# Performance work log

Hardware: AMD Instinct MI355X
Metric: run time of the kernel (lower is better)

## Reference

```python
import jax, jax.numpy as jnp
import numpy as np

NEG_SLOPE = 0.01  # torch nn.LeakyReLU default


def setup_inputs() -> dict:
    key = jax.random.key(0)
    k1, k2, k3, k4, k5 = jax.random.split(key, 5)
    B, C, N, O = 32, 512, 1024, 512
    x = jax.random.normal(k1, (B, C, N), dtype=jnp.float32)
    wq = jax.random.normal(k2, (C,), dtype=jnp.float32) * (1.0 / np.sqrt(C))
    wk = jax.random.normal(k3, (C,), dtype=jnp.float32) * (1.0 / np.sqrt(C))
    wm = jax.random.normal(k4, (O, C), dtype=jnp.float32) * (1.0 / np.sqrt(C))
    bm = jax.random.normal(k5, (O,), dtype=jnp.float32) * 0.01
    return {"x": x, "wq": wq, "wk": wk, "wm": wm, "bm": bm}


def reference(x, wq, wk, wm, bm):
    # x: [B, C, N]
    q = jnp.einsum('c,bcn->bn', wq, x)            # [B, N] (Conv1d C->1, k=1, no bias)
    k = jnp.einsum('c,bcn->bn', wk, x)            # [B, N]
    scores = q[:, None, :] + k[:, :, None]        # [B, N, N] additive broadcast
    scores = jnp.where(scores > 0, scores, NEG_SLOPE * scores)  # LeakyReLU
    att = jax.nn.softmax(scores, axis=-1)         # softmax over last dim
    agg = jnp.einsum('bcn,bmn->bcm', x, att)      # weighted aggregation [B, C, N]
    out = jnp.einsum('oc,bcm->bom', wm, agg) + bm[None, :, None]  # Conv1d k=1
    return jax.nn.relu(out)
```

## Files before the change

### kernel.cpp

```cpp
#include <hip/hip_runtime.h>


constexpr int B = 32, C = 512, N = 1024, O = 512;
constexpr float L2E = 1.4426950408889634f;

typedef _Float16 half8 __attribute__((ext_vector_type(8)));
typedef _Float16 half4v __attribute__((ext_vector_type(4)));
typedef _Float16 half2v __attribute__((ext_vector_type(2)));
typedef float f32x4 __attribute__((ext_vector_type(4)));
typedef float f32x16 __attribute__((ext_vector_type(16)));

#if __has_builtin(__builtin_amdgcn_exp2f)
#define EXP2(x) __builtin_amdgcn_exp2f(x)
#else
#define EXP2(x) exp2f(x)
#endif

__device__ __forceinline__ half8 cvt8(float4 a, float4 b) {
  half8 h;
  h[0] = (_Float16)a.x; h[1] = (_Float16)a.y; h[2] = (_Float16)a.z; h[3] = (_Float16)a.w;
  h[4] = (_Float16)b.x; h[5] = (_Float16)b.y; h[6] = (_Float16)b.z; h[7] = (_Float16)b.w;
  return h;
}

__device__ __forceinline__ void gload16(const _Float16* g, _Float16* l) {
  __builtin_amdgcn_global_load_lds(
      (const __attribute__((address_space(1))) unsigned int*)(g),
      (__attribute__((address_space(3))) unsigned int*)(l), 16, 0, 0);
}

__global__ __launch_bounds__(256) void prep_kernel(const float* __restrict__ x,
    const float* __restrict__ wq, const float* __restrict__ wk,
    const float* __restrict__ wm,
    float* __restrict__ q, float* __restrict__ k,
    _Float16* __restrict__ wmh, _Float16* __restrict__ xhT) {
  __shared__ half2v Ts[32 * 67];
  int b  = blockIdx.y;
  int n0 = blockIdx.x * 64;
  int t = threadIdx.x;

  if (blockIdx.x == 0) {
    const float* wsrc = wm + b * 8192;
    _Float16* wdst = wmh + b * 8192;
#pragma unroll
    for (int j = 0; j < 4; ++j) {
      int i = j * 2048 + t * 8;
      float4 a = *(const float4*)(wsrc + i);
      float4 bb = *(const float4*)(wsrc + i + 4);
      *(half8*)(wdst + i) = cvt8(a, bb);
    }
  }

  int cp = t >> 3;
  int ng = t & 7;
  const float* xbase = x + ((size_t)b * C + 2 * cp) * N + n0 + ng * 8;
  int nl = t >> 2;
  int hq = t & 3;
  _Float16* xout = xhT + ((size_t)b * N + n0 + nl) * C + hq * 16;
  float aq[8] = {}, ak[8] = {};

  for (int ch = 0; ch < 8; ++ch) {
    int c0 = ch * 64;
    const float* xr = xbase + (size_t)c0 * N;
    float4 a0 = *(const float4*)(xr);
    float4 a1 = *(const float4*)(xr + 4);
    float4 b0 = *(const float4*)(xr + N);
    float4 b1 = *(const float4*)(xr + N + 4);
    float2 wq2 = *(const float2*)&wq[c0 + 2 * cp];
    float2 wk2 = *(const float2*)&wk[c0 + 2 * cp];
    aq[0] = fmaf(wq2.x, a0.x, fmaf(wq2.y, b0.x, aq[0]));
    aq[1] = fmaf(wq2.x, a0.y, fmaf(wq2.y, b0.y, aq[1]));
    aq[2] = fmaf(wq2.x, a0.z, fmaf(wq2.y, b0.z, aq[2]));
    aq[3] = fmaf(wq2.x, a0.w, fmaf(wq2.y, b0.w, aq[3]));
    aq[4] = fmaf(wq2.x, a1.x, fmaf(wq2.y, b1.x, aq[4]));
    aq[5] = fmaf(wq2.x, a1.y, fmaf(wq2.y, b1.y, aq[5]));
    aq[6] = fmaf(wq2.x, a1.z, fmaf(wq2.y, b1.z, aq[6]));
    aq[7] = fmaf(wq2.x, a1.w, fmaf(wq2.y, b1.w, aq[7]));
    ak[0] = fmaf(wk2.x, a0.x, fmaf(wk2.y, b0.x, ak[0]));
    ak[1] = fmaf(wk2.x, a0.y, fmaf(wk2.y, b0.y, ak[1]));
    ak[2] = fmaf(wk2.x, a0.z, fmaf(wk2.y, b0.z, ak[2]));
    ak[3] = fmaf(wk2.x, a0.w, fmaf(wk2.y, b0.w, ak[3]));
    ak[4] = fmaf(wk2.x, a1.x, fmaf(wk2.y, b1.x, ak[4]));
    ak[5] = fmaf(wk2.x, a1.y, fmaf(wk2.y, b1.y, ak[5]));
    ak[6] = fmaf(wk2.x, a1.z, fmaf(wk2.y, b1.z, ak[6]));
    ak[7] = fmaf(wk2.x, a1.w, fmaf(wk2.y, b1.w, ak[7]));
    {
      half2v* xp = &Ts[cp * 67 + ng * 8];
      xp[0] = half2v{(_Float16)a0.x, (_Float16)b0.x};
      xp[1] = half2v{(_Float16)a0.y, (_Float16)b0.y};
      xp[2] = half2v{(_Float16)a0.z, (_Float16)b0.z};
      xp[3] = half2v{(_Float16)a0.w, (_Float16)b0.w};
      xp[4] = half2v{(_Float16)a1.x, (_Float16)b1.x};
      xp[5] = half2v{(_Float16)a1.y, (_Float16)b1.y};
      xp[6] = half2v{(_Float16)a1.z, (_Float16)b1.z};
      xp[7] = half2v{(_Float16)a1.w, (_Float16)b1.w};
    }
    __syncthreads();
    half8 o0h, o1h;
#pragma unroll
    for (int u = 0; u < 4; ++u) {
      half2v pr = Ts[(hq * 8 + u) * 67 + nl];
      o0h[2 * u] = pr[0]; o0h[2 * u + 1] = pr[1];
    }
#pragma unroll
    for (int u = 4; u < 8; ++u) {
      half2v pr = Ts[(hq * 8 + u) * 67 + nl];
      o1h[2 * (u - 4)] = pr[0]; o1h[2 * (u - 4) + 1] = pr[1];
    }
    *(half8*)(xout + c0)     = o0h;
    *(half8*)(xout + c0 + 8) = o1h;
    __syncthreads();
  }

  float* red = (float*)Ts;
#pragma unroll
  for (int j = 0; j < 8; ++j) red[cp * 67 + ng * 8 + j] = aq[j];
  __syncthreads();
  if (t < 64) {
    float s = 0.f;
#pragma unroll
    for (int p = 0; p < 32; ++p) s += red[p * 67 + t];
    q[b * N + n0 + t] = L2E * s;
  }
  __syncthreads();
#pragma unroll
  for (int j = 0; j < 8; ++j) red[cp * 67 + ng * 8 + j] = ak[j];
  __syncthreads();
  if (t < 64) {
    float s = 0.f;
#pragma unroll
    for (int p = 0; p < 32; ++p) s += red[p * 67 + t];
    k[b * N + n0 + t] = L2E * s;
  }
}

__global__ __launch_bounds__(256) void gemm_y_kernel(const _Float16* __restrict__ xhT,
    const _Float16* __restrict__ wmh, _Float16* __restrict__ Yt) {
  __shared__ __align__(16) _Float16 As[2][128 * 32];
  int f = blockIdx.x;
  int xcd = f & 7, g = f >> 3;
  int o_id = g & 3;
  int p2 = xcd * 32 + (g >> 2);
  int n_id = p2 & 7, b = p2 >> 3;
  int n0 = n_id * 128, o0 = o_id * 128;
  int t = threadIdx.x;
  int w = t >> 6, l = t & 63;
  int nw = w >> 1, ow = w & 1;
  int lm = l & 15, q8 = (l >> 4) * 8, q4 = (l >> 4) * 4;

  const _Float16* asrc[2];
#pragma unroll
  for (int m = 0; m < 2; ++m) {
    int u = m * 256 + t;
    asrc[m] = xhT + ((size_t)b * N + n0 + (u >> 2)) * C + (u & 3) * 8;
  }
  const _Float16* wb[4];
#pragma unroll
  for (int j = 0; j < 4; ++j)
    wb[j] = wmh + (size_t)(o0 + ow * 64 + j * 16 + lm) * C + q8;

#pragma unroll
  for (int m = 0; m < 2; ++m)
    gload16(asrc[m], &As[0][(m * 256 + (t & ~63)) * 8]);
  __syncthreads();

  f32x4 acc[4][4] = {};
  for (int it = 0; it < 16; ++it) {
    int p = it & 1;
    if (it < 15) {
      int c1 = (it + 1) * 32;
#pragma unroll
      for (int m = 0; m < 2; ++m)
        gload16(asrc[m] + c1, &As[p ^ 1][(m * 256 + (t & ~63)) * 8]);
    }
    int c0 = it * 32;
    half8 bf[4];
#pragma unroll
    for (int j = 0; j < 4; ++j) bf[j] = *(const half8*)(wb[j] + c0);
#pragma unroll
    for (int i = 0; i < 4; ++i) {
      half8 af = *(const half8*)&As[p][(nw * 64 + i * 16 + lm) * 32 + q8];
#pragma unroll
      for (int j = 0; j < 4; ++j)
        acc[i][j] = __builtin_amdgcn_mfma_f32_16x16x32_f16(af, bf[j], acc[i][j], 0, 0, 0);
    }
    __syncthreads();
  }

#pragma unroll
  for (int i = 0; i < 4; ++i) {
    int n_b = n0 + nw * 64 + i * 16 + q4;
#pragma unroll
    for (int j = 0; j < 4; ++j) {
      int o_c = o0 + ow * 64 + j * 16 + lm;
      half4v h;
      h[0] = (_Float16)acc[i][j][0];
      h[1] = (_Float16)acc[i][j][1];
      h[2] = (_Float16)acc[i][j][2];
      h[3] = (_Float16)acc[i][j][3];
      *(half4v*)&Yt[((size_t)b * O + o_c) * N + n_b] = h;
    }
  }
}

__global__ __launch_bounds__(512) void gemm_out_kernel(const _Float16* __restrict__ Yt,
    const float* __restrict__ q, const float* __restrict__ k,
    const float* __restrict__ bm, float* __restrict__ out) {
  __shared__ __align__(16) float qs[N];
  __shared__ __align__(16) _Float16 Ys[2][256 * 40];
  __shared__ float izs[256];
  __shared__ float mred[8];
  int b  = blockIdx.y;
  int o0 = blockIdx.x * 256;
  int m0 = blockIdx.z * 256;
  int t = threadIdx.x;
  int w = t >> 6, l = t & 63;
  int ml = l & 31, g2 = l >> 5;

  float2 q2 = *(const float2*)&q[b * N + t * 2];
  *(float2*)&qs[t * 2] = q2;
  float lmax = fmaxf(q2.x, q2.y);
#pragma unroll
  for (int off = 32; off > 0; off >>= 1) lmax = fmaxf(lmax, __shfl_down(lmax, off, 64));
  if (l == 0) mred[w] = lmax;

  float km = k[b * N + m0 + w * 32 + ml];

  half8 ones;
#pragma unroll
  for (int jj = 0; jj < 8; ++jj) ones[jj] = (_Float16)1.0f;
  f32x16 acc_z = {};
  int yr = t >> 1, yp = t & 1;
  const _Float16* ysrc = Yt + ((size_t)b * O + o0 + yr) * N + yp * 16;

  {
    half8 z0 = *(const half8*)(ysrc);
    half8 z1 = *(const half8*)(ysrc + 8);
    *(half8*)&Ys[0][yr * 40 + yp * 16]     = z0;
    *(half8*)&Ys[0][yr * 40 + yp * 16 + 8] = z1;
  }
  __syncthreads();

  float qmv = mred[0];
#pragma unroll
  for (int j = 1; j < 8; ++j) qmv = fmaxf(qmv, mred[j]);
  float s0 = qmv + km;
  float M  = fmaxf(s0, 0.01f * s0);
  float kc2 = km - M;
  float kc3 = fmaf(0.01f, km, -M);

  f32x16 acc[8] = {};
  for (int it = 0; it < N / 32; ++it) {
    int p = it & 1;
    int n0k = it * 32;
    half8 z0, z1;
    if (it < N / 32 - 1) {
      z0 = *(const half8*)(ysrc + n0k + 32);
      z1 = *(const half8*)(ysrc + n0k + 40);
    }
#pragma unroll
    for (int kh = 0; kh < 2; ++kh) {
      float4 qa = *(const float4*)&qs[n0k + kh * 16 + g2 * 8];
      float4 qb = *(const float4*)&qs[n0k + kh * 16 + g2 * 8 + 4];
      float qv[8] = {qa.x, qa.y, qa.z, qa.w, qb.x, qb.y, qb.z, qb.w};
      half8 af;
#pragma unroll
      for (int jj = 0; jj < 8; ++jj) {
        float arg = fmaxf(qv[jj] + kc2, fmaf(0.01f, qv[jj], kc3));
        af[jj] = (_Float16)EXP2(arg);
      }
      acc_z = __builtin_amdgcn_mfma_f32_32x32x16_f16(af, ones, acc_z, 0, 0, 0);
#pragma unroll
      for (int s = 0; s < 8; ++s) {
        half8 bf = *(const half8*)&Ys[p][(s * 32 + ml) * 40 + kh * 16 + g2 * 8];
        acc[s] = __builtin_amdgcn_mfma_f32_32x32x16_f16(af, bf, acc[s], 0, 0, 0);
      }
    }
    if (it < N / 32 - 1) {
      *(half8*)&Ys[p ^ 1][yr * 40 + yp * 16]     = z0;
      *(half8*)&Ys[p ^ 1][yr * 40 + yp * 16 + 8] = z1;
    }
    __syncthreads();
  }

  if (ml == 0) {
#pragma unroll
    for (int rq = 0; rq < 4; ++rq)
#pragma unroll
      for (int r = 0; r < 4; ++r)
        izs[w * 32 + r + 8 * rq + 4 * g2] = 1.0f / acc_z[rq * 4 + r];
  }
  __syncthreads();

  float4 izv[4];
#pragma unroll
  for (int rq = 0; rq < 4; ++rq)
    izv[rq] = *(const float4*)&izs[w * 32 + 8 * rq + 4 * g2];

#pragma unroll
  for (int s = 0; s < 8; ++s) {
    int o_c = o0 + s * 32 + ml;
    float bias = bm[o_c];
#pragma unroll
    for (int rq = 0; rq < 4; ++rq) {
      int m_b = m0 + w * 32 + 8 * rq + 4 * g2;
      float4 r;
      r.x = fmaxf(fmaf(acc[s][rq * 4 + 0], izv[rq].x, bias), 0.f);
      r.y = fmaxf(fmaf(acc[s][rq * 4 + 1], izv[rq].y, bias), 0.f);
      r.z = fmaxf(fmaf(acc[s][rq * 4 + 2], izv[rq].z, bias), 0.f);
      r.w = fmaxf(fmaf(acc[s][rq * 4 + 3], izv[rq].w, bias), 0.f);
      *(float4*)&out[((size_t)b * O + o_c) * N + m_b] = r;
    }
  }
}

extern "C" void kernel_launch(void* const* d_in, const int* in_sizes, int n_in,
                              void* d_out, int out_size, void* d_ws, size_t ws_size,
                              hipStream_t stream) {
  const float* x  = (const float*)d_in[0];
  const float* wq = (const float*)d_in[1];
  const float* wk = (const float*)d_in[2];
  const float* wm = (const float*)d_in[3];
  const float* bm = (const float*)d_in[4];
  float* out = (float*)d_out;

  float* q    = (float*)d_ws;
  float* k    = q + B * N;
  _Float16* wmh = (_Float16*)(k + B * N + 64);
  _Float16* Yt  = wmh + (size_t)O * C;
  _Float16* xhT = (_Float16*)d_out;

  prep_kernel<<<dim3(N / 64, B), 256, 0, stream>>>(x, wq, wk, wm, q, k, wmh, xhT);
  gemm_y_kernel<<<dim3(1024), 256, 0, stream>>>(xhT, wmh, Yt);
  gemm_out_kernel<<<dim3(O / 256, B, N / 256), 512, 0, stream>>>(Yt, q, k, bm, out);
}
```

Before: 209.7 us.

## Fuse three kernels into one cooperative persistent kernel with grid syncs

```diff
diff --git a/kernel.cpp b/kernel.cpp
--- a/kernel.cpp
+++ b/kernel.cpp
@@ -1,4 +1,7 @@
 #include <hip/hip_runtime.h>
+#include <hip/hip_cooperative_groups.h>
+
+namespace cg = cooperative_groups;
 
 
 constexpr int B = 32, C = 512, N = 1024, O = 512;
@@ -29,287 +32,296 @@
       (__attribute__((address_space(3))) unsigned int*)(l), 16, 0, 0);
 }
 
-__global__ __launch_bounds__(256) void prep_kernel(const float* __restrict__ x,
-    const float* __restrict__ wq, const float* __restrict__ wk,
-    const float* __restrict__ wm,
-    float* __restrict__ q, float* __restrict__ k,
-    _Float16* __restrict__ wmh, _Float16* __restrict__ xhT) {
-  __shared__ half2v Ts[32 * 67];
-  int b  = blockIdx.y;
-  int n0 = blockIdx.x * 64;
+__global__ __launch_bounds__(512) void fused_kernel(
+    const float* __restrict__ x, const float* __restrict__ wq,
+    const float* __restrict__ wk, const float* __restrict__ wm,
+    const float* __restrict__ bm, float* __restrict__ q, float* __restrict__ k,
+    float* __restrict__ qpart, _Float16* __restrict__ wmh,
+    _Float16* __restrict__ xhT, _Float16* __restrict__ Yt,
+    float* __restrict__ out) {
+  __shared__ __align__(16) unsigned char smem[46080];
+  cg::grid_group grid = cg::this_grid();
+  int bb = blockIdx.x;
   int t = threadIdx.x;
 
-  if (blockIdx.x == 0) {
-    const float* wsrc = wm + b * 8192;
-    _Float16* wdst = wmh + b * 8192;
-#pragma unroll
-    for (int j = 0; j < 4; ++j) {
-      int i = j * 2048 + t * 8;
+  {
+    int su = t >> 8, tp = t & 255;
+    half2v* Tu = (half2v*)smem + su * (32 * 67);
+    int unit = bb * 2 + su;
+    int b = unit >> 4, n0 = (unit & 15) * 64;
+
+    if (bb < 64) {
+      int i = t * 8;
+      const float* wsrc = wm + bb * 4096;
       float4 a = *(const float4*)(wsrc + i);
-      float4 bb = *(const float4*)(wsrc + i + 4);
-      *(half8*)(wdst + i) = cvt8(a, bb);
+      float4 b4 = *(const float4*)(wsrc + i + 4);
+      *(half8*)(wmh + bb * 4096 + i) = cvt8(a, b4);
+    }
+
+    int cp = tp >> 3;
+    int ng = tp & 7;
+    const float* xbase = x + ((size_t)b * C + 2 * cp) * N + n0 + ng * 8;
+    int nl = tp >> 2;
+    int hq = tp & 3;
+    _Float16* xout = xhT + ((size_t)b * N + n0 + nl) * C + hq * 16;
+    float aq[8] = {}, ak[8] = {};
+
+    for (int ch = 0; ch < 8; ++ch) {
+      int c0 = ch * 64;
+      const float* xr = xbase + (size_t)c0 * N;
+      float4 a0 = *(const float4*)(xr);
+      float4 a1 = *(const float4*)(xr + 4);
+      float4 b0 = *(const float4*)(xr + N);
+      float4 b1 = *(const float4*)(xr + N + 4);
+      float2 wq2 = *(const float2*)&wq[c0 + 2 * cp];
+      float2 wk2 = *(const float2*)&wk[c0 + 2 * cp];
+      aq[0] = fmaf(wq2.x, a0.x, fmaf(wq2.y, b0.x, aq[0]));
+      aq[1] = fmaf(wq2.x, a0.y, fmaf(wq2.y, b0.y, aq[1]));
+      aq[2] = fmaf(wq2.x, a0.z, fmaf(wq2.y, b0.z, aq[2]));
+      aq[3] = fmaf(wq2.x, a0.w, fmaf(wq2.y, b0.w, aq[3]));
+      aq[4] = fmaf(wq2.x, a1.x, fmaf(wq2.y, b1.x, aq[4]));
+      aq[5] = fmaf(wq2.x, a1.y, fmaf(wq2.y, b1.y, aq[5]));
+      aq[6] = fmaf(wq2.x, a1.z, fmaf(wq2.y, b1.z, aq[6]));
+      aq[7] = fmaf(wq2.x, a1.w, fmaf(wq2.y, b1.w, aq[7]));
+      ak[0] = fmaf(wk2.x, a0.x, fmaf(wk2.y, b0.x, ak[0]));
+      ak[1] = fmaf(wk2.x, a0.y, fmaf(wk2.y, b0.y, ak[1]));
+      ak[2] = fmaf(wk2.x, a0.z, fmaf(wk2.y, b0.z, ak[2]));
+      ak[3] = fmaf(wk2.x, a0.w, fmaf(wk2.y, b0.w, ak[3]));
+      ak[4] = fmaf(wk2.x, a1.x, fmaf(wk2.y, b1.x, ak[4]));
+      ak[5] = fmaf(wk2.x, a1.y, fmaf(wk2.y, b1.y, ak[5]));
+      ak[6] = fmaf(wk2.x, a1.z, fmaf(wk2.y, b1.z, ak[6]));
+      ak[7] = fmaf(wk2.x, a1.w, fmaf(wk2.y, b1.w, ak[7]));
+      {
+        half2v* xp = &Tu[cp * 67 + ng * 8];
+        xp[0] = half2v{(_Float16)a0.x, (_Float16)b0.x};
+        xp[1] = half2v{(_Float16)a0.y, (_Float16)b0.y};
+        xp[2] = half2v{(_Float16)a0.z, (_Float16)b0.z};
+        xp[3] = half2v{(_Float16)a0.w, (_Float16)b0.w};
+        xp[4] = half2v{(_Float16)a1.x, (_Float16)b1.x};
+        xp[5] = half2v{(_Float16)a1.y, (_Float16)b1.y};
+        xp[6] = half2v{(_Float16)a1.z, (_Float16)b1.z};
+        xp[7] = half2v{(_Float16)a1.w, (_Float16)b1.w};
+      }
+      __syncthreads();
+      half8 o0h, o1h;
+#pragma unroll
+      for (int u = 0; u < 4; ++u) {
+        half2v pr = Tu[(hq * 8 + u) * 67 + nl];
+        o0h[2 * u] = pr[0]; o0h[2 * u + 1] = pr[1];
+      }
+#pragma unroll
+      for (int u = 4; u < 8; ++u) {
+        half2v pr = Tu[(hq * 8 + u) * 67 + nl];
+        o1h[2 * (u - 4)] = pr[0]; o1h[2 * (u - 4) + 1] = pr[1];
+      }
+      *(half8*)(xout + c0)     = o0h;
+      *(half8*)(xout + c0 + 8) = o1h;
+      __syncthreads();
+    }
+
+    float* red = (float*)Tu;
+#pragma unroll
+    for (int j = 0; j < 8; ++j) red[cp * 67 + ng * 8 + j] = aq[j];
+    __syncthreads();
+    if (tp < 64) {
+      float s = 0.f;
+#pragma unroll
+      for (int p = 0; p < 32; ++p) s += red[p * 67 + tp];
+      float qv = L2E * s;
+      q[b * N + n0 + tp] = qv;
+      float lm2 = qv;
+#pragma unroll
+      for (int off = 32; off > 0; off >>= 1)
+        lm2 = fmaxf(lm2, __shfl_down(lm2, off, 64));
+      if ((t & 63) == 0) qpart[unit] = lm2;
+    }
+    __syncthreads();
+#pragma unroll
+    for (int j = 0; j < 8; ++j) red[cp * 67 + ng * 8 + j] = ak[j];
+    __syncthreads();
+    if (tp < 64) {
+      float s = 0.f;
+#pragma unroll
+      for (int p = 0; p < 32; ++p) s += red[p * 67 + tp];
+      k[b * N + n0 + tp] = L2E * s;
     }
   }
-
-  int cp = t >> 3;
-  int ng = t & 7;
-  const float* xbase = x + ((size_t)b * C + 2 * cp) * N + n0 + ng * 8;
-  int nl = t >> 2;
-  int hq = t & 3;
-  _Float16* xout = xhT + ((size_t)b * N + n0 + nl) * C + hq * 16;
-  float aq[8] = {}, ak[8] = {};
-
-  for (int ch = 0; ch < 8; ++ch) {
-    int c0 = ch * 64;
-    const float* xr = xbase + (size_t)c0 * N;
-    float4 a0 = *(const float4*)(xr);
-    float4 a1 = *(const float4*)(xr + 4);
-    float4 b0 = *(const float4*)(xr + N);
-    float4 b1 = *(const float4*)(xr + N + 4);
-    float2 wq2 = *(const float2*)&wq[c0 + 2 * cp];
-    float2 wk2 = *(const float2*)&wk[c0 + 2 * cp];
-    aq[0] = fmaf(wq2.x, a0.x, fmaf(wq2.y, b0.x, aq[0]));
-    aq[1] = fmaf(wq2.x, a0.y, fmaf(wq2.y, b0.y, aq[1]));
-    aq[2] = fmaf(wq2.x, a0.z, fmaf(wq2.y, b0.z, aq[2]));
-    aq[3] = fmaf(wq2.x, a0.w, fmaf(wq2.y, b0.w, aq[3]));
-    aq[4] = fmaf(wq2.x, a1.x, fmaf(wq2.y, b1.x, aq[4]));
-    aq[5] = fmaf(wq2.x, a1.y, fmaf(wq2.y, b1.y, aq[5]));
-    aq[6] = fmaf(wq2.x, a1.z, fmaf(wq2.y, b1.z, aq[6]));
-    aq[7] = fmaf(wq2.x, a1.w, fmaf(wq2.y, b1.w, aq[7]));
-    ak[0] = fmaf(wk2.x, a0.x, fmaf(wk2.y, b0.x, ak[0]));
-    ak[1] = fmaf(wk2.x, a0.y, fmaf(wk2.y, b0.y, ak[1]));
-    ak[2] = fmaf(wk2.x, a0.z, fmaf(wk2.y, b0.z, ak[2]));
-    ak[3] = fmaf(wk2.x, a0.w, fmaf(wk2.y, b0.w, ak[3]));
-    ak[4] = fmaf(wk2.x, a1.x, fmaf(wk2.y, b1.x, ak[4]));
-    ak[5] = fmaf(wk2.x, a1.y, fmaf(wk2.y, b1.y, ak[5]));
-    ak[6] = fmaf(wk2.x, a1.z, fmaf(wk2.y, b1.z, ak[6]));
-    ak[7] = fmaf(wk2.x, a1.w, fmaf(wk2.y, b1.w, ak[7]));
+  __threadfence();
+  grid.sync();
+
+  {
+    int su = t >> 8, tp = t & 255;
+    _Float16* Asu = (_Float16*)smem + su * (2 * 128 * 32);
+    int w = tp >> 6, l = tp & 63;
+    int nw = w >> 1, ow = w & 1;
+    int lm = l & 15, q8 = (l >> 4) * 8, q4 = (l >> 4) * 4;
+    int xcd = bb & 7;
+
+    for (int rep = 0; rep < 2; ++rep) {
+      int g = (bb >> 3) * 4 + rep * 2 + su;
+      int o_id = g & 3;
+      int p2 = xcd * 32 + (g >> 2);
+      int n_id = p2 & 7, by = p2 >> 3;
+      int n0 = n_id * 128, o0 = o_id * 128;
+
+      const _Float16* asrc[2];
+#pragma unroll
+      for (int m = 0; m < 2; ++m) {
+        int u = m * 256 + tp;
+        asrc[m] = xhT + ((size_t)by * N + n0 + (u >> 2)) * C + (u & 3) * 8;
+      }
+      const _Float16* wb[4];
+#pragma unroll
+      for (int j = 0; j < 4; ++j)
+        wb[j] = wmh + (size_t)(o0 + ow * 64 + j * 16 + lm) * C + q8;
+
+#pragma unroll
+      for (int m = 0; m < 2; ++m)
+        gload16(asrc[m], &Asu[(m * 256 + (tp & ~63)) * 8]);
+      __syncthreads();
+
+      f32x4 acc[4][4] = {};
+      for (int it = 0; it < 16; ++it) {
+        int p = it & 1;
+        if (it < 15) {
+          int c1 = (it + 1) * 32;
+#pragma unroll
+          for (int m = 0; m < 2; ++m)
+            gload16(asrc[m] + c1, &Asu[(p ^ 1) * 4096 + (m * 256 + (tp & ~63)) * 8]);
+        }
+        int c0 = it * 32;
+        half8 bf[4];
+#pragma unroll
+        for (int j = 0; j < 4; ++j) bf[j] = *(const half8*)(wb[j] + c0);
+#pragma unroll
+        for (int i = 0; i < 4; ++i) {
+          half8 af = *(const half8*)&Asu[p * 4096 + (nw * 64 + i * 16 + lm) * 32 + q8];
+#pragma unroll
+          for (int j = 0; j < 4; ++j)
+            acc[i][j] = __builtin_amdgcn_mfma_f32_16x16x32_f16(af, bf[j], acc[i][j], 0, 0, 0);
+        }
+        __syncthreads();
+      }
+
+#pragma unroll
+      for (int i = 0; i < 4; ++i) {
+        int n_b = n0 + nw * 64 + i * 16 + q4;
+#pragma unroll
+        for (int j = 0; j < 4; ++j) {
+          int o_c = o0 + ow * 64 + j * 16 + lm;
+          half4v h;
+          h[0] = (_Float16)acc[i][j][0];
+          h[1] = (_Float16)acc[i][j][1];
+          h[2] = (_Float16)acc[i][j][2];
+          h[3] = (_Float16)acc[i][j][3];
+          *(half4v*)&Yt[((size_t)by * O + o_c) * N + n_b] = h;
+        }
+      }
+      __syncthreads();
+    }
+  }
+  __threadfence();
+  grid.sync();
+
+  {
+    float* qs = (float*)smem;
+    _Float16* Ys = (_Float16*)(smem + 4096);
+    float* izs = (float*)(smem + 4096 + 40960);
+    int xcd = bb & 7, w2 = bb >> 3;
+    int pairLocal = w2 >> 2, m_id = w2 & 3;
+    int pair = xcd * 8 + pairLocal;
+    int o_id = pair & 1, by = pair >> 1;
+    int o0 = o_id * 256, m0 = m_id * 256;
+    int w = t >> 6, l = t & 63;
+    int ml = l & 31, g2 = l >> 5;
+
+    *(float2*)&qs[t * 2] = *(const float2*)&q[by * N + t * 2];
+    float qmv = qpart[by * 16];
+#pragma unroll
+    for (int j = 1; j < 16; ++j) qmv = fmaxf(qmv, qpart[by * 16 + j]);
+    float km = k[by * N + m0 + w * 32 + ml];
+    float s0 = qmv + km;
+    float M  = fmaxf(s0, 0.01f * s0);
+    float kc2 = km - M;
+    float kc3 = fmaf(0.01f, km, -M);
+
+    half8 ones;
+#pragma unroll
+    for (int jj = 0; jj < 8; ++jj) ones[jj] = (_Float16)1.0f;
+    f32x16 acc_z = {};
+    int yr = t >> 1, yp = t & 1;
+    const _Float16* ysrc = Yt + ((size_t)by * O + o0 + yr) * N + yp * 16;
+
     {
-      half2v* xp = &Ts[cp * 67 + ng * 8];
-      xp[0] = half2v{(_Float16)a0.x, (_Float16)b0.x};
-      xp[1] = half2v{(_Float16)a0.y, (_Float16)b0.y};
-      xp[2] = half2v{(_Float16)a0.z, (_Float16)b0.z};
-      xp[3] = half2v{(_Float16)a0.w, (_Float16)b0.w};
-      xp[4] = half2v{(_Float16)a1.x, (_Float16)b1.x};
-      xp[5] = half2v{(_Float16)a1.y, (_Float16)b1.y};
-      xp[6] = half2v{(_Float16)a1.z, (_Float16)b1.z};
-      xp[7] = half2v{(_Float16)a1.w, (_Float16)b1.w};
-    }
-    __syncthreads();
-    half8 o0h, o1h;
-#pragma unroll
-    for (int u = 0; u < 4; ++u) {
-      half2v pr = Ts[(hq * 8 + u) * 67 + nl];
-      o0h[2 * u] = pr[0]; o0h[2 * u + 1] = pr[1];
-    }
-#pragma unroll
-    for (int u = 4; u < 8; ++u) {
-      half2v pr = Ts[(hq * 8 + u) * 67 + nl];
-      o1h[2 * (u - 4)] = pr[0]; o1h[2 * (u - 4) + 1] = pr[1];
-    }
-    *(half8*)(xout + c0)     = o0h;
-    *(half8*)(xout + c0 + 8) = o1h;
-    __syncthreads();
-  }
-
-  float* red = (float*)Ts;
-#pragma unroll
-  for (int j = 0; j < 8; ++j) red[cp * 67 + ng * 8 + j] = aq[j];
-  __syncthreads();
-  if (t < 64) {
-    float s = 0.f;
-#pragma unroll
-    for (int p = 0; p < 32; ++p) s += red[p * 67 + t];
-    q[b * N + n0 + t] = L2E * s;
-  }
-  __syncthreads();
-#pragma unroll
-  for (int j = 0; j < 8; ++j) red[cp * 67 + ng * 8 + j] = ak[j];
-  __syncthreads();
-  if (t < 64) {
-    float s = 0.f;
-#pragma unroll
-    for (int p = 0; p < 32; ++p) s += red[p * 67 + t];
-    k[b * N + n0 + t] = L2E * s;
-  }
-}
-
-__global__ __launch_bounds__(256) void gemm_y_kernel(const _Float16* __restrict__ xhT,
-    const _Float16* __restrict__ wmh, _Float16* __restrict__ Yt) {
-  __shared__ __align__(16) _Float16 As[2][128 * 32];
-  int f = blockIdx.x;
-  int xcd = f & 7, g = f >> 3;
-  int o_id = g & 3;
-  int p2 = xcd * 32 + (g >> 2);
-  int n_id = p2 & 7, b = p2 >> 3;
-  int n0 = n_id * 128, o0 = o_id * 128;
-  int t = threadIdx.x;
-  int w = t >> 6, l = t & 63;
-  int nw = w >> 1, ow = w & 1;
-  int lm = l & 15, q8 = (l >> 4) * 8, q4 = (l >> 4) * 4;
-
-  const _Float16* asrc[2];
-#pragma unroll
-  for (int m = 0; m < 2; ++m) {
-    int u = m * 256 + t;
-    asrc[m] = xhT + ((size_t)b * N + n0 + (u >> 2)) * C + (u & 3) * 8;
-  }
-  const _Float16* wb[4];
-#pragma unroll
-  for (int j = 0; j < 4; ++j)
-    wb[j] = wmh + (size_t)(o0 + ow * 64 + j * 16 + lm) * C + q8;
-
-#pragma unroll
-  for (int m = 0; m < 2; ++m)
-    gload16(asrc[m], &As[0][(m * 256 + (t & ~63)) * 8]);
-  __syncthreads();
-
-  f32x4 acc[4][4] = {};
-  for (int it = 0; it < 16; ++it) {
-    int p = it & 1;
-    if (it < 15) {
-      int c1 = (it + 1) * 32;
-#pragma unroll
-      for (int m = 0; m < 2; ++m)
-        gload16(asrc[m] + c1, &As[p ^ 1][(m * 256 + (t & ~63)) * 8]);
-    }
-    int c0 = it * 32;
-    half8 bf[4];
-#pragma unroll
-    for (int j = 0; j < 4; ++j) bf[j] = *(const half8*)(wb[j] + c0);
-#pragma unroll
-    for (int i = 0; i < 4; ++i) {
-      half8 af = *(const half8*)&As[p][(nw * 64 + i * 16 + lm) * 32 + q8];
-#pragma unroll
-      for (int j = 0; j < 4; ++j)
-        acc[i][j] = __builtin_amdgcn_mfma_f32_16x16x32_f16(af, bf[j], acc[i][j], 0, 0, 0);
-    }
-    __syncthreads();
-  }
-
-#pragma unroll
-  for (int i = 0; i < 4; ++i) {
-    int n_b = n0 + nw * 64 + i * 16 + q4;
-#pragma unroll
-    for (int j = 0; j < 4; ++j) {
-      int o_c = o0 + ow * 64 + j * 16 + lm;
-      half4v h;
-      h[0] = (_Float16)acc[i][j][0];
-      h[1] = (_Float16)acc[i][j][1];
-      h[2] = (_Float16)acc[i][j][2];
-      h[3] = (_Float16)acc[i][j][3];
-      *(half4v*)&Yt[((size_t)b * O + o_c) * N + n_b] = h;
-    }
-  }
-}
-
-__global__ __launch_bounds__(512) void gemm_out_kernel(const _Float16* __restrict__ Yt,
-    const float* __restrict__ q, const float* __restrict__ k,
-    const float* __restrict__ bm, float* __restrict__ out) {
-  __shared__ __align__(16) float qs[N];
-  __shared__ __align__(16) _Float16 Ys[2][256 * 40];
-  __shared__ float izs[256];
-  __shared__ float mred[8];
-  int b  = blockIdx.y;
-  int o0 = blockIdx.x * 256;
-  int m0 = blockIdx.z * 256;
-  int t = threadIdx.x;
-  int w = t >> 6, l = t & 63;
-  int ml = l & 31, g2 = l >> 5;
-
-  float2 q2 = *(const float2*)&q[b * N + t * 2];
-  *(float2*)&qs[t * 2] = q2;
-  float lmax = fmaxf(q2.x, q2.y);
-#pragma unroll
-  for (int off = 32; off > 0; off >>= 1) lmax = fmaxf(lmax, __shfl_down(lmax, off, 64));
-  if (l == 0) mred[w] = lmax;
-
-  float km = k[b * N + m0 + w * 32 + ml];
-
-  half8 ones;
-#pragma unroll
-  for (int jj = 0; jj < 8; ++jj) ones[jj] = (_Float16)1.0f;
-  f32x16 acc_z = {};
-  int yr = t >> 1, yp = t & 1;
-  const _Float16* ysrc = Yt + ((size_t)b * O + o0 + yr) * N + yp * 16;
-
-  {
-    half8 z0 = *(const half8*)(ysrc);
-    half8 z1 = *(const half8*)(ysrc + 8);
-    *(half8*)&Ys[0][yr * 40 + yp * 16]     = z0;
-    *(half8*)&Ys[0][yr * 40 + yp * 16 + 8] = z1;
-  }
-  __syncthreads();
-
-  float qmv = mred[0];
-#pragma unroll
-  for (int j = 1; j < 8; ++j) qmv = fmaxf(qmv, mred[j]);
-  float s0 = qmv + km;
-  float M  = fmaxf(s0, 0.01f * s0);
-  float kc2 = km - M;
-  float kc3 = fmaf(0.01f, km, -M);
-
-  f32x16 acc[8] = {};
-  for (int it = 0; it < N / 32; ++it) {
-    int p = it & 1;
-    int n0k = it * 32;
-    half8 z0, z1;
-    if (it < N / 32 - 1) {
-      z0 = *(const half8*)(ysrc + n0k + 32);
-      z1 = *(const half8*)(ysrc + n0k + 40);
-    }
-#pragma unroll
-    for (int kh = 0; kh < 2; ++kh) {
-      float4 qa = *(const float4*)&qs[n0k + kh * 16 + g2 * 8];
-      float4 qb = *(const float4*)&qs[n0k + kh * 16 + g2 * 8 + 4];
-      float qv[8] = {qa.x, qa.y, qa.z, qa.w, qb.x, qb.y, qb.z, qb.w};
-      half8 af;
-#pragma unroll
-      for (int jj = 0; jj < 8; ++jj) {
-        float arg = fmaxf(qv[jj] + kc2, fmaf(0.01f, qv[jj], kc3));
-        af[jj] = (_Float16)EXP2(arg);
-      }
-      acc_z = __builtin_amdgcn_mfma_f32_32x32x16_f16(af, ones, acc_z, 0, 0, 0);
-#pragma unroll
-      for (int s = 0; s < 8; ++s) {
-        half8 bf = *(const half8*)&Ys[p][(s * 32 + ml) * 40 + kh * 16 + g2 * 8];
-        acc[s] = __builtin_amdgcn_mfma_f32_32x32x16_f16(af, bf, acc[s], 0, 0, 0);
-      }
-    }
-    if (it < N / 32 - 1) {
-      *(half8*)&Ys[p ^ 1][yr * 40 + yp * 16]     = z0;
-      *(half8*)&Ys[p ^ 1][yr * 40 + yp * 16 + 8] = z1;
-    }
-    __syncthreads();
-  }
-
-  if (ml == 0) {
+      half8 z0 = *(const half8*)(ysrc);
+      half8 z1 = *(const half8*)(ysrc + 8);
+      *(half8*)&Ys[yr * 40 + yp * 16]     = z0;
+      *(half8*)&Ys[yr * 40 + yp * 16 + 8] = z1;
+    }
+    __syncthreads();
+
+    f32x16 acc[8] = {};
+    for (int it = 0; it < N / 32; ++it) {
+      int p = it & 1;
+      int n0k = it * 32;
+      half8 z0, z1;
+      if (it < N / 32 - 1) {
+        z0 = *(const half8*)(ysrc + n0k + 32);
+        z1 = *(const half8*)(ysrc + n0k + 40);
+      }
+#pragma unroll
+      for (int kh = 0; kh < 2; ++kh) {
+        float4 qa = *(const float4*)&qs[n0k + kh * 16 + g2 * 8];
+        float4 qb = *(const float4*)&qs[n0k + kh * 16 + g2 * 8 + 4];
+        float qv[8] = {qa.x, qa.y, qa.z, qa.w, qb.x, qb.y, qb.z, qb.w};
+        half8 af;
+#pragma unroll
+        for (int jj = 0; jj < 8; ++jj) {
+          float arg = fmaxf(qv[jj] + kc2, fmaf(0.01f, qv[jj], kc3));
+          af[jj] = (_Float16)EXP2(arg);
+        }
+        acc_z = __builtin_amdgcn_mfma_f32_32x32x16_f16(af, ones, acc_z, 0, 0, 0);
+#pragma unroll
+        for (int s = 0; s < 8; ++s) {
+          half8 bf = *(const half8*)&Ys[p * 10240 + (s * 32 + ml) * 40 + kh * 16 + g2 * 8];
+          acc[s] = __builtin_amdgcn_mfma_f32_32x32x16_f16(af, bf, acc[s], 0, 0, 0);
+        }
+      }
+      if (it < N / 32 - 1) {
+        *(half8*)&Ys[(p ^ 1) * 10240 + yr * 40 + yp * 16]     = z0;
+        *(half8*)&Ys[(p ^ 1) * 10240 + yr * 40 + yp * 16 + 8] = z1;
+      }
+      __syncthreads();
+    }
+
+    if (ml == 0) {
+#pragma unroll
+      for (int rq = 0; rq < 4; ++rq)
+#pragma unroll
+        for (int r = 0; r < 4; ++r)
+          izs[w * 32 + r + 8 * rq + 4 * g2] = 1.0f / acc_z[rq * 4 + r];
+    }
+    __syncthreads();
+
+    float4 izv[4];
 #pragma unroll
     for (int rq = 0; rq < 4; ++rq)
-#pragma unroll
-      for (int r = 0; r < 4; ++r)
-        izs[w * 32 + r + 8 * rq + 4 * g2] = 1.0f / acc_z[rq * 4 + r];
-  }
-  __syncthreads();
-
-  float4 izv[4];
-#pragma unroll
-  for (int rq = 0; rq < 4; ++rq)
-    izv[rq] = *(const float4*)&izs[w * 32 + 8 * rq + 4 * g2];
-
-#pragma unroll
-  for (int s = 0; s < 8; ++s) {
-    int o_c = o0 + s * 32 + ml;
-    float bias = bm[o_c];
-#pragma unroll
-    for (int rq = 0; rq < 4; ++rq) {
-      int m_b = m0 + w * 32 + 8 * rq + 4 * g2;
-      float4 r;
-      r.x = fmaxf(fmaf(acc[s][rq * 4 + 0], izv[rq].x, bias), 0.f);
-      r.y = fmaxf(fmaf(acc[s][rq * 4 + 1], izv[rq].y, bias), 0.f);
-      r.z = fmaxf(fmaf(acc[s][rq * 4 + 2], izv[rq].z, bias), 0.f);
-      r.w = fmaxf(fmaf(acc[s][rq * 4 + 3], izv[rq].w, bias), 0.f);
-      *(float4*)&out[((size_t)b * O + o_c) * N + m_b] = r;
+      izv[rq] = *(const float4*)&izs[w * 32 + 8 * rq + 4 * g2];
+
+#pragma unroll
+    for (int s = 0; s < 8; ++s) {
+      int o_c = o0 + s * 32 + ml;
+      float bias = bm[o_c];
+#pragma unroll
+      for (int rq = 0; rq < 4; ++rq) {
+        int m_b = m0 + w * 32 + 8 * rq + 4 * g2;
+        float4 r;
+        r.x = fmaxf(fmaf(acc[s][rq * 4 + 0], izv[rq].x, bias), 0.f);
+        r.y = fmaxf(fmaf(acc[s][rq * 4 + 1], izv[rq].y, bias), 0.f);
+        r.z = fmaxf(fmaf(acc[s][rq * 4 + 2], izv[rq].z, bias), 0.f);
+        r.w = fmaxf(fmaf(acc[s][rq * 4 + 3], izv[rq].w, bias), 0.f);
+        *(float4*)&out[((size_t)by * O + o_c) * N + m_b] = r;
+      }
     }
   }
 }
@@ -324,13 +336,16 @@
   const float* bm = (const float*)d_in[4];
   float* out = (float*)d_out;
 
-  float* q    = (float*)d_ws;
-  float* k    = q + B * N;
-  _Float16* wmh = (_Float16*)(k + B * N + 64);
+  float* q     = (float*)d_ws;
+  float* k     = q + B * N;
+  float* qpart = k + B * N;
+  _Float16* wmh = (_Float16*)(qpart + 512);
   _Float16* Yt  = wmh + (size_t)O * C;
   _Float16* xhT = (_Float16*)d_out;
 
-  prep_kernel<<<dim3(N / 64, B), 256, 0, stream>>>(x, wq, wk, wm, q, k, wmh, xhT);
-  gemm_y_kernel<<<dim3(1024), 256, 0, stream>>>(xhT, wmh, Yt);
-  gemm_out_kernel<<<dim3(O / 256, B, N / 256), 512, 0, stream>>>(Yt, q, k, bm, out);
+  void* args[] = {(void*)&x, (void*)&wq, (void*)&wk, (void*)&wm, (void*)&bm,
+                  (void*)&q, (void*)&k, (void*)&qpart, (void*)&wmh,
+                  (void*)&xhT, (void*)&Yt, (void*)&out};
+  hipLaunchCooperativeKernel((const void*)fused_kernel, dim3(256), dim3(512),
+                             args, 0, stream);
 }
```

Measured after the change: 415.9 us. 1.98x slower.
